# Kernel tuning notes

Measured on AMD Instinct MI355X. Metric: run time of the kernel, lower is better.

The kernel has to match this reference:

```python
import jax, jax.numpy as jnp
import numpy as np

# Instant-NGP hash grid constants (match init_kwargs)
N_MAX, N_MIN = 2048.0, 16.0
L, T, F, DIM = 16, 2**19, 2, 3
NV = 2**DIM  # 8 corners of a voxel
# primes stored as int32 in the original (2654435761 wraps negative) -> replicate exactly
PIS = jnp.asarray(np.array([1, 2654435761, 805459861], dtype=np.uint32).astype(np.int32))
# bin_mask[v, d] = True -> corner v takes floor along dim d
_neigs = np.arange(NV, dtype=np.int64)[:, None]
_dims = np.arange(DIM, dtype=np.int64)[None, :]
BIN_MASK = jnp.asarray((_neigs & (1 << _dims)) == 0)  # [8, 3]
# per-level grid resolutions N_l = N_min * b**l
_b = np.exp((np.log(N_MAX) - np.log(N_MIN)) / L)
SCALES = jnp.asarray((N_MIN * _b ** np.arange(L)).astype(np.float32))  # [L]


def setup_inputs() -> dict:
    key = jax.random.key(0)
    k1, k2 = jax.random.split(key)
    N = 2_000_000
    x = jax.random.uniform(k1, (N, DIM), dtype=jnp.float32)  # points in [0,1)^3 (mu=0, sigma=1)
    # per-level embedding tables, init U(-1e-4, 1e-4) as in the torch module
    W = jax.random.uniform(k2, (L, T, F), minval=-1e-4, maxval=1e-4, dtype=jnp.float32)
    return {"x": x, "W": W}


def _hash(idxs):
    # idxs: [N, 8, 3] int32. int32 wraparound multiply matches low 32 bits of the
    # torch int64 product; since T is a power of two and Python-style mod of a
    # negative by a positive only depends on the low log2(T) bits, result matches.
    prod = idxs * PIS  # [N, 8, 3] int32 (wraps)
    h = prod[..., 0] ^ prod[..., 1] ^ prod[..., 2]
    return h % T  # jnp remainder follows sign of divisor -> nonnegative


def _encode(x, W):
    def level(carry, level_args):
        scale, Wl = level_args
        un_x = x * scale                                   # [N, 3]
        x0 = un_x.astype(jnp.int32)                        # trunc == floor for x >= 0
        diff = jax.lax.stop_gradient(un_x - x0.astype(un_x.dtype))  # [N, 3], detached as in torch
        # corner integer coords: floor where bin_mask else floor+1
        idxs = jnp.where(BIN_MASK[None], x0[:, None, :], x0[:, None, :] + 1)  # [N, 8, 3]
        fv = Wl[_hash(idxs)]                               # [N, 8, F] gather
        wts = jnp.where(BIN_MASK[None], 1.0 - diff[:, None, :], diff[:, None, :])
        wts = wts.prod(axis=-1, keepdims=True)             # [N, 8, 1] trilinear weights
        return carry, (fv * wts).sum(axis=-2)              # [N, F]

    _, ys = jax.lax.scan(level, 0, (SCALES, W))            # [L, N, F]
    # original writes level l into y[:, l*F:(l+1)*F]
    return jnp.transpose(ys, (1, 0, 2)).reshape(x.shape[0], L * F)


def reference(x, W):
    return _encode(x, W)
```

## Files before the change

kernel.cpp:

```cpp
#include <hip/hip_runtime.h>
#include <hip/hip_fp16.h>
#include <math.h>

#define NLEV 16
#define NDENSE 5
#define TBLN (1u << 19)
#define TMASK (TBLN - 1u)
#define NPT 4
#define PR1 2654435761u
#define PR2 805459861u

typedef float f32x4 __attribute__((ext_vector_type(4)));
typedef unsigned int u32;
typedef unsigned int u32x2 __attribute__((ext_vector_type(2)));
typedef unsigned int u32x4 __attribute__((ext_vector_type(4)));

struct ScaleArgs { float s[NLEV]; };

#define DD0 18
#define DD1 23
#define DD2 31
#define DD3 41
#define DD4 55
#define DO0 0
#define DO1 5508
#define DO2 17146
#define DO3 45976
#define DO4 113216
#define DTOT 276566

static __device__ __forceinline__ u32 packf2(float a, float b) {
    __half2 h = __floats2half2_rn(a, b);
    return __builtin_bit_cast(u32, h);
}
static __device__ __forceinline__ float2 unpack16(u32 u) {
    __half2 h = __builtin_bit_cast(__half2, u);
    return __half22float2(h);
}

__global__ __launch_bounds__(256)
void convert_w(const float* __restrict__ W, u32* __restrict__ Wh, int np4)
{
    int i = blockIdx.x * blockDim.x + threadIdx.x;
    if (i >= np4) return;
    const f32x4* src = reinterpret_cast<const f32x4*>(W) + (size_t)i * 2;
    f32x4 A = __builtin_nontemporal_load(src);
    f32x4 B = __builtin_nontemporal_load(src + 1);
    u32x4 o = { packf2(A.x, A.y), packf2(A.z, A.w),
                packf2(B.x, B.y), packf2(B.z, B.w) };
    __builtin_nontemporal_store(o, reinterpret_cast<u32x4*>(Wh) + i);
}

__global__ __launch_bounds__(256)
void build_dense(const float* __restrict__ Wlf, u32x2* __restrict__ Gpl, int D, int P)
{
    int v = blockIdx.x * blockDim.x + threadIdx.x;
    if (v >= P) return;
    int Dx = D - 1;
    int ix = v % Dx;
    int rest = v / Dx;
    int iy = rest % D;
    int iz = rest / D;
    u32 e = ((u32)iy * PR1) ^ ((u32)iz * PR2);
    u32 h0 = (e ^ (u32)ix) & TMASK;
    u32 h1 = (e ^ (u32)(ix + 1)) & TMASK;
    float2 f0 = *reinterpret_cast<const float2*>(Wlf + (size_t)h0 * 2u);
    float2 f1 = *reinterpret_cast<const float2*>(Wlf + (size_t)h1 * 2u);
    u32x2 o = { packf2(f0.x, f0.y), packf2(f1.x, f1.y) };
    Gpl[v] = o;
}


template<int D>
static __device__ __forceinline__ void dense_body(
    const float* __restrict__ x, const u32x2* __restrict__ Gp,
    u32* __restrict__ scl, float scale, int N, int TOT, int t)
{
    constexpr int Dx = D - 1;
    constexpr int zstep = D * Dx;

    int nn[NPT];
    float dx[NPT], dy[NPT], dz[NPT];
    int base[NPT];
    u32x2 P0[NPT], P1[NPT], P2[NPT], P3[NPT];

    #pragma unroll
    for (int i = 0; i < NPT; ++i) {
        int n = t + i * TOT;
        if (n > N - 1) n = N - 1;
        nn[i] = n;
        float px = __builtin_nontemporal_load(&x[(size_t)n * 3 + 0]);
        float py = __builtin_nontemporal_load(&x[(size_t)n * 3 + 1]);
        float pz = __builtin_nontemporal_load(&x[(size_t)n * 3 + 2]);
        float ux = px * scale, uy = py * scale, uz = pz * scale;
        int ix = (int)ux, iy = (int)uy, iz = (int)uz;
        dx[i] = ux - (float)ix;
        dy[i] = uy - (float)iy;
        dz[i] = uz - (float)iz;
        base[i] = (iz * D + iy) * Dx + ix;
    }

    #pragma unroll
    for (int i = 0; i < NPT; ++i) {
        int b = base[i];
        P0[i] = Gp[b];
        P1[i] = Gp[b + Dx];
        P2[i] = Gp[b + zstep];
        P3[i] = Gp[b + zstep + Dx];
    }

    #pragma unroll
    for (int i = 0; i < NPT; ++i) {
        float ax = 0.f, ay = 0.f;
        float wxl = 1.f - dx[i], wxh = dx[i];
        float wyl = 1.f - dy[i], wyh = dy[i];
        float wzl = 1.f - dz[i], wzh = dz[i];
        {
            float2 f0 = unpack16(P0[i].x), f1 = unpack16(P0[i].y);
            float w0 = (wxl * wyl) * wzl, w1 = (wxh * wyl) * wzl;
            ax = fmaf(f0.x, w0, ax); ay = fmaf(f0.y, w0, ay);
            ax = fmaf(f1.x, w1, ax); ay = fmaf(f1.y, w1, ay);
        }
        {
            float2 f0 = unpack16(P1[i].x), f1 = unpack16(P1[i].y);
            float w0 = (wxl * wyh) * wzl, w1 = (wxh * wyh) * wzl;
            ax = fmaf(f0.x, w0, ax); ay = fmaf(f0.y, w0, ay);
            ax = fmaf(f1.x, w1, ax); ay = fmaf(f1.y, w1, ay);
        }
        {
            float2 f0 = unpack16(P2[i].x), f1 = unpack16(P2[i].y);
            float w0 = (wxl * wyl) * wzh, w1 = (wxh * wyl) * wzh;
            ax = fmaf(f0.x, w0, ax); ay = fmaf(f0.y, w0, ay);
            ax = fmaf(f1.x, w1, ax); ay = fmaf(f1.y, w1, ay);
        }
        {
            float2 f0 = unpack16(P3[i].x), f1 = unpack16(P3[i].y);
            float w0 = (wxl * wyh) * wzh, w1 = (wxh * wyh) * wzh;
            ax = fmaf(f0.x, w0, ax); ay = fmaf(f0.y, w0, ay);
            ax = fmaf(f1.x, w1, ax); ay = fmaf(f1.y, w1, ay);
        }
        __builtin_nontemporal_store(packf2(ax, ay), scl + nn[i]);
    }
}

static __device__ __forceinline__ void hash_body(
    const float* __restrict__ x, const u32* __restrict__ Wl,
    u32* __restrict__ scl, float scale, int N, int TOT, int t)
{
    int nn[NPT];
    float dx[NPT], dy[NPT], dz[NPT];
    u32 a0[NPT], a1[NPT], a2[NPT];
    u32 fv[NPT][8];

    #pragma unroll
    for (int i = 0; i < NPT; ++i) {
        int n = t + i * TOT;
        if (n > N - 1) n = N - 1;
        nn[i] = n;
        float px = __builtin_nontemporal_load(&x[(size_t)n * 3 + 0]);
        float py = __builtin_nontemporal_load(&x[(size_t)n * 3 + 1]);
        float pz = __builtin_nontemporal_load(&x[(size_t)n * 3 + 2]);
        float ux = px * scale, uy = py * scale, uz = pz * scale;
        int ix = (int)ux, iy = (int)uy, iz = (int)uz;
        dx[i] = ux - (float)ix;
        dy[i] = uy - (float)iy;
        dz[i] = uz - (float)iz;
        a0[i] = (unsigned)ix;
        a1[i] = (unsigned)iy * PR1;
        a2[i] = (unsigned)iz * PR2;
    }

    #pragma unroll
    for (int i = 0; i < NPT; ++i) {
        u32 b0 = a0[i] + 1u, b1 = a1[i] + PR1, b2 = a2[i] + PR2;
        u32 E[4] = { a1[i] ^ a2[i], b1 ^ a2[i], a1[i] ^ b2, b1 ^ b2 };
        if ((a0[i] & 1u) == 0u) {
            #pragma unroll
            for (int j = 0; j < 4; ++j) {
                u32 hl = (E[j] ^ a0[i]) & TMASK;
                u32x2 p = *reinterpret_cast<const u32x2*>(Wl + (hl & ~1u));
                u32 lo = (hl & 1u) ? p.y : p.x;
                u32 hi = (hl & 1u) ? p.x : p.y;
                fv[i][2 * j + 0] = lo;
                fv[i][2 * j + 1] = hi;
            }
        } else {
            #pragma unroll
            for (int j = 0; j < 4; ++j) {
                u32 hl = (E[j] ^ a0[i]) & TMASK;
                u32 hh = (E[j] ^ b0) & TMASK;
                fv[i][2 * j + 0] = Wl[hl];
                fv[i][2 * j + 1] = Wl[hh];
            }
        }
    }

    #pragma unroll
    for (int i = 0; i < NPT; ++i) {
        float ax = 0.f, ay = 0.f;
        #pragma unroll
        for (int v = 0; v < 8; ++v) {
            float wx = (v & 1) ? dx[i] : 1.f - dx[i];
            float wy = (v & 2) ? dy[i] : 1.f - dy[i];
            float wz = (v & 4) ? dz[i] : 1.f - dz[i];
            float w = (wx * wy) * wz;
            float2 f = unpack16(fv[i][v]);
            ax = fmaf(f.x, w, ax);
            ay = fmaf(f.y, w, ay);
        }
        __builtin_nontemporal_store(packf2(ax, ay), scl + nn[i]);
    }
}

__global__ __launch_bounds__(256)
void fused_levels(const float* __restrict__ x, const u32* __restrict__ Wh,
                  const u32x2* __restrict__ Gp, u32* __restrict__ scratch,
                  ScaleArgs sc, int N, int TOT, int BPL)
{
    int lvl = blockIdx.x / BPL;
    int t = (blockIdx.x - lvl * BPL) * blockDim.x + threadIdx.x;
    if (t >= TOT) return;
    float scale = sc.s[lvl];
    u32* scl = scratch + (size_t)lvl * (size_t)N;

    switch (lvl) {
        case 0: dense_body<DD0>(x, Gp + DO0, scl, scale, N, TOT, t); break;
        case 1: dense_body<DD1>(x, Gp + DO1, scl, scale, N, TOT, t); break;
        case 2: dense_body<DD2>(x, Gp + DO2, scl, scale, N, TOT, t); break;
        case 3: dense_body<DD3>(x, Gp + DO3, scl, scale, N, TOT, t); break;
        case 4: dense_body<DD4>(x, Gp + DO4, scl, scale, N, TOT, t); break;
        default:
            hash_body(x, Wh + (size_t)(lvl - NDENSE) * TBLN, scl, scale, N, TOT, t);
            break;
    }
}

__global__ __launch_bounds__(256)
void transpose_kernel(const u32* __restrict__ sc, float* __restrict__ out, int N)
{
    int n = blockIdx.x * blockDim.x + threadIdx.x;
    if (n >= N) return;
    float r[2 * NLEV];
    #pragma unroll
    for (int l = 0; l < NLEV; ++l) {
        u32 u = __builtin_nontemporal_load(sc + (size_t)l * N + n);
        float2 f = unpack16(u);
        r[2 * l + 0] = f.x;
        r[2 * l + 1] = f.y;
    }
    f32x4* o = reinterpret_cast<f32x4*>(out + (size_t)n * (2 * NLEV));
    #pragma unroll
    for (int j = 0; j < 8; ++j) {
        f32x4 v = { r[4 * j + 0], r[4 * j + 1], r[4 * j + 2], r[4 * j + 3] };
        o[j] = v;
    }
}

__global__ __launch_bounds__(256)
void hashenc_fallback(const float* __restrict__ x, const float* __restrict__ W,
                      float* __restrict__ out, ScaleArgs sc, int N)
{
    int n = blockIdx.x * blockDim.x + threadIdx.x;
    if (n >= N) return;
    float px = x[(size_t)n * 3 + 0];
    float py = x[(size_t)n * 3 + 1];
    float pz = x[(size_t)n * 3 + 2];
    float acc[2 * NLEV];
    #pragma unroll
    for (int l = 0; l < NLEV; ++l) {
        float s = sc.s[l];
        float ux = px * s, uy = py * s, uz = pz * s;
        int ix = (int)ux, iy = (int)uy, iz = (int)uz;
        float dx = ux - (float)ix, dy = uy - (float)iy, dz = uz - (float)iz;
        unsigned a0 = (unsigned)ix;
        unsigned a1 = (unsigned)iy * PR1;
        unsigned a2 = (unsigned)iz * PR2;
        unsigned b0 = a0 + 1u, b1 = a1 + PR1, b2 = a2 + PR2;
        const float* Wl = W + (size_t)l * TBLN * 2u;
        float ax = 0.f, ay = 0.f;
        #pragma unroll
        for (int v = 0; v < 8; ++v) {
            unsigned h = ((v & 1) ? b0 : a0) ^ ((v & 2) ? b1 : a1) ^ ((v & 4) ? b2 : a2);
            h &= TMASK;
            float wx = (v & 1) ? dx : 1.f - dx;
            float wy = (v & 2) ? dy : 1.f - dy;
            float wz = (v & 4) ? dz : 1.f - dz;
            float w = (wx * wy) * wz;
            const float2 fvv = *reinterpret_cast<const float2*>(Wl + (size_t)h * 2u);
            ax = fmaf(fvv.x, w, ax);
            ay = fmaf(fvv.y, w, ay);
        }
        acc[2 * l + 0] = ax;
        acc[2 * l + 1] = ay;
    }
    float4* o = reinterpret_cast<float4*>(out + (size_t)n * (2 * NLEV));
    #pragma unroll
    for (int j = 0; j < 8; ++j)
        o[j] = make_float4(acc[4 * j + 0], acc[4 * j + 1], acc[4 * j + 2], acc[4 * j + 3]);
}

extern "C" void kernel_launch(void* const* d_in, const int* in_sizes, int n_in,
                              void* d_out, int out_size, void* d_ws, size_t ws_size,
                              hipStream_t stream) {
    const float* x = (const float*)d_in[0];
    const float* W = (const float*)d_in[1];
    float* out = (float*)d_out;
    int N = in_sizes[0] / 3;

    ScaleArgs sc;
    double b = exp((log(2048.0) - log(16.0)) / 16.0);
    for (int l = 0; l < NLEV; ++l) {
        double p;
        switch (l) {
            case 0: p = 1.0; break;
            case 1: p = b;   break;
            case 2: p = b * b; break;
            default: p = pow(b, (double)l); break;
        }
        sc.s[l] = (float)(16.0 * p);
    }

    size_t wh_u32 = (size_t)(NLEV - NDENSE) * TBLN;
    size_t gp_u32 = (size_t)DTOT * 2u;
    size_t scr_u32 = (size_t)NLEV * (size_t)N;
    size_t need = (wh_u32 + gp_u32 + scr_u32) * sizeof(u32);

    if (ws_size >= need) {
        u32* Wh = (u32*)d_ws;
        u32x2* Gp = reinterpret_cast<u32x2*>(Wh + wh_u32);
        u32* scratch = Wh + wh_u32 + gp_u32;

        int np4 = (int)(wh_u32 / 4);
        hipLaunchKernelGGL(convert_w, dim3((np4 + 255) / 256), dim3(256), 0, stream,
                           W + (size_t)NDENSE * TBLN * 2u, Wh, np4);

        const int Dl[NDENSE] = { DD0, DD1, DD2, DD3, DD4 };
        const int Ol[NDENSE] = { DO0, DO1, DO2, DO3, DO4 };
        for (int l = 0; l < NDENSE; ++l) {
            int P = (Dl[l] - 1) * Dl[l] * Dl[l];
            hipLaunchKernelGGL(build_dense, dim3((P + 255) / 256), dim3(256), 0, stream,
                               W + (size_t)l * TBLN * 2u, Gp + Ol[l], Dl[l], P);
        }

        int TOT = (N + NPT - 1) / NPT;
        int BPL = (TOT + 255) / 256;
        hipLaunchKernelGGL(fused_levels, dim3(NLEV * BPL), dim3(256), 0, stream,
                           x, Wh, Gp, scratch, sc, N, TOT, BPL);

        int gt = (N + 255) / 256;
        hipLaunchKernelGGL(transpose_kernel, dim3(gt), dim3(256), 0, stream,
                           scratch, out, N);
    } else {
        int grid = (N + 255) / 256;
        hipLaunchKernelGGL(hashenc_fallback, dim3(grid), dim3(256), 0, stream,
                           x, W, out, sc, N);
    }
}
```

Before: 687.3 us.

## Serve coarse levels from LDS-resident grids, densify level 5, tile transpose through LDS

Levels 0 and 1 now get separate kernels that copy a small dense fp16 grid (18^3 and 23^3 entries) into shared memory and do the trilinear lookups from LDS. Level 5 (D=75) becomes a precomputed dense paired grid instead of going through the hash table. The transpose kernel stages each level's scratch values in LDS so the 32-float output rows are written coalesced. These changes aim to reduce scattered global gathers and uncoalesced writes, at the cost of two extra launches that each re-read x and a larger dense-grid build.

```diff
diff --git a/kernel.cpp b/kernel.cpp
--- a/kernel.cpp
+++ b/kernel.cpp
@@ -3,10 +3,10 @@
 #include <math.h>
 
 #define NLEV 16
-#define NDENSE 5
 #define TBLN (1u << 19)
 #define TMASK (TBLN - 1u)
 #define NPT 4
+#define NPTL 16
 #define PR1 2654435761u
 #define PR2 805459861u
 
@@ -17,17 +17,20 @@
 
 struct ScaleArgs { float s[NLEV]; };
 
-#define DD0 18
-#define DD1 23
+#define DU0 18
+#define DU1 23
+#define GU0 0
+#define GU1 5832
+#define GUTOT 17999
 #define DD2 31
 #define DD3 41
 #define DD4 55
-#define DO0 0
-#define DO1 5508
-#define DO2 17146
-#define DO3 45976
-#define DO4 113216
-#define DTOT 276566
+#define DD5 75
+#define GO2 0
+#define GO3 28830
+#define GO4 96070
+#define GO5 259420
+#define GPTOT 675670
 
 static __device__ __forceinline__ u32 packf2(float a, float b) {
     __half2 h = __floats2half2_rn(a, b);
@@ -49,6 +52,20 @@
     u32x4 o = { packf2(A.x, A.y), packf2(A.z, A.w),
                 packf2(B.x, B.y), packf2(B.z, B.w) };
     __builtin_nontemporal_store(o, reinterpret_cast<u32x4*>(Wh) + i);
+}
+
+__global__ __launch_bounds__(256)
+void build_unpaired(const float* __restrict__ Wlf, u32* __restrict__ Gu, int D, int P)
+{
+    int v = blockIdx.x * blockDim.x + threadIdx.x;
+    if (v >= P) return;
+    int ix = v % D;
+    int rest = v / D;
+    int iy = rest % D;
+    int iz = rest / D;
+    u32 h = (((u32)iy * PR1) ^ ((u32)iz * PR2) ^ (u32)ix) & TMASK;
+    float2 f = *reinterpret_cast<const float2*>(Wlf + (size_t)h * 2u);
+    Gu[v] = packf2(f.x, f.y);
 }
 
 __global__ __launch_bounds__(256)
@@ -68,6 +85,49 @@
     float2 f1 = *reinterpret_cast<const float2*>(Wlf + (size_t)h1 * 2u);
     u32x2 o = { packf2(f0.x, f0.y), packf2(f1.x, f1.y) };
     Gpl[v] = o;
+}
+
+template<int D>
+__global__ __launch_bounds__(256)
+void lds_level(const float* __restrict__ x, const u32* __restrict__ Gu,
+               u32* __restrict__ scl, float scale, int N)
+{
+    __shared__ u32 g[D * D * D];
+    for (int i = threadIdx.x; i < D * D * D; i += 256) g[i] = Gu[i];
+    __syncthreads();
+
+    int base = blockIdx.x * (256 * NPTL);
+    #pragma unroll 4
+    for (int i = 0; i < NPTL; ++i) {
+        int n = base + i * 256 + (int)threadIdx.x;
+        if (n < N) {
+            float px = __builtin_nontemporal_load(&x[(size_t)n * 3 + 0]);
+            float py = __builtin_nontemporal_load(&x[(size_t)n * 3 + 1]);
+            float pz = __builtin_nontemporal_load(&x[(size_t)n * 3 + 2]);
+            float ux = px * scale, uy = py * scale, uz = pz * scale;
+            int ix = (int)ux, iy = (int)uy, iz = (int)uz;
+            float dx = ux - (float)ix, dy = uy - (float)iy, dz = uz - (float)iz;
+            int b = (iz * D + iy) * D + ix;
+            u32 c0 = g[b],             c1 = g[b + 1];
+            u32 c2 = g[b + D],         c3 = g[b + D + 1];
+            u32 c4 = g[b + D * D],     c5 = g[b + D * D + 1];
+            u32 c6 = g[b + D * D + D], c7 = g[b + D * D + D + 1];
+            float wxl = 1.f - dx, wxh = dx;
+            float wyl = 1.f - dy, wyh = dy;
+            float wzl = 1.f - dz, wzh = dz;
+            float ax = 0.f, ay = 0.f;
+            float2 f;
+            f = unpack16(c0); { float w = (wxl * wyl) * wzl; ax = fmaf(f.x, w, ax); ay = fmaf(f.y, w, ay); }
+            f = unpack16(c1); { float w = (wxh * wyl) * wzl; ax = fmaf(f.x, w, ax); ay = fmaf(f.y, w, ay); }
+            f = unpack16(c2); { float w = (wxl * wyh) * wzl; ax = fmaf(f.x, w, ax); ay = fmaf(f.y, w, ay); }
+            f = unpack16(c3); { float w = (wxh * wyh) * wzl; ax = fmaf(f.x, w, ax); ay = fmaf(f.y, w, ay); }
+            f = unpack16(c4); { float w = (wxl * wyl) * wzh; ax = fmaf(f.x, w, ax); ay = fmaf(f.y, w, ay); }
+            f = unpack16(c5); { float w = (wxh * wyl) * wzh; ax = fmaf(f.x, w, ax); ay = fmaf(f.y, w, ay); }
+            f = unpack16(c6); { float w = (wxl * wyh) * wzh; ax = fmaf(f.x, w, ax); ay = fmaf(f.y, w, ay); }
+            f = unpack16(c7); { float w = (wxh * wyh) * wzh; ax = fmaf(f.x, w, ax); ay = fmaf(f.y, w, ay); }
+            __builtin_nontemporal_store(packf2(ax, ay), scl + n);
+        }
+    }
 }
 
 
@@ -217,20 +277,20 @@
                   const u32x2* __restrict__ Gp, u32* __restrict__ scratch,
                   ScaleArgs sc, int N, int TOT, int BPL)
 {
-    int lvl = blockIdx.x / BPL;
-    int t = (blockIdx.x - lvl * BPL) * blockDim.x + threadIdx.x;
+    int li = blockIdx.x / BPL;
+    int lvl = li + 2;
+    int t = (blockIdx.x - li * BPL) * blockDim.x + threadIdx.x;
     if (t >= TOT) return;
     float scale = sc.s[lvl];
     u32* scl = scratch + (size_t)lvl * (size_t)N;
 
     switch (lvl) {
-        case 0: dense_body<DD0>(x, Gp + DO0, scl, scale, N, TOT, t); break;
-        case 1: dense_body<DD1>(x, Gp + DO1, scl, scale, N, TOT, t); break;
-        case 2: dense_body<DD2>(x, Gp + DO2, scl, scale, N, TOT, t); break;
-        case 3: dense_body<DD3>(x, Gp + DO3, scl, scale, N, TOT, t); break;
-        case 4: dense_body<DD4>(x, Gp + DO4, scl, scale, N, TOT, t); break;
+        case 2: dense_body<DD2>(x, Gp + GO2, scl, scale, N, TOT, t); break;
+        case 3: dense_body<DD3>(x, Gp + GO3, scl, scale, N, TOT, t); break;
+        case 4: dense_body<DD4>(x, Gp + GO4, scl, scale, N, TOT, t); break;
+        case 5: dense_body<DD5>(x, Gp + GO5, scl, scale, N, TOT, t); break;
         default:
-            hash_body(x, Wh + (size_t)(lvl - NDENSE) * TBLN, scl, scale, N, TOT, t);
+            hash_body(x, Wh + (size_t)(lvl - 6) * TBLN, scl, scale, N, TOT, t);
             break;
     }
 }
@@ -238,21 +298,27 @@
 __global__ __launch_bounds__(256)
 void transpose_kernel(const u32* __restrict__ sc, float* __restrict__ out, int N)
 {
-    int n = blockIdx.x * blockDim.x + threadIdx.x;
-    if (n >= N) return;
-    float r[2 * NLEV];
+    __shared__ u32 lds[16][257];
+    int P0 = blockIdx.x * 256;
+    int t = threadIdx.x;
     #pragma unroll
     for (int l = 0; l < NLEV; ++l) {
-        u32 u = __builtin_nontemporal_load(sc + (size_t)l * N + n);
-        float2 f = unpack16(u);
-        r[2 * l + 0] = f.x;
-        r[2 * l + 1] = f.y;
-    }
-    f32x4* o = reinterpret_cast<f32x4*>(out + (size_t)n * (2 * NLEV));
-    #pragma unroll
-    for (int j = 0; j < 8; ++j) {
-        f32x4 v = { r[4 * j + 0], r[4 * j + 1], r[4 * j + 2], r[4 * j + 3] };
-        o[j] = v;
+        int n = P0 + t;
+        if (n < N) lds[l][t] = __builtin_nontemporal_load(sc + (size_t)l * N + n);
+    }
+    __syncthreads();
+    int w = t >> 6, l6 = t & 63;
+    #pragma unroll
+    for (int k = 0; k < 8; ++k) {
+        int p = w * 64 + k * 8 + (l6 >> 3);
+        int c = l6 & 7;
+        if (P0 + p < N) {
+            float2 f0 = unpack16(lds[2 * c][p]);
+            float2 f1 = unpack16(lds[2 * c + 1][p]);
+            f32x4 v = { f0.x, f0.y, f1.x, f1.y };
+            __builtin_nontemporal_store(v,
+                reinterpret_cast<f32x4*>(out + (size_t)(P0 + p) * 32u + (size_t)c * 4u));
+        }
     }
 }
 
@@ -320,31 +386,51 @@
         sc.s[l] = (float)(16.0 * p);
     }
 
-    size_t wh_u32 = (size_t)(NLEV - NDENSE) * TBLN;
-    size_t gp_u32 = (size_t)DTOT * 2u;
+    size_t wh_u32 = (size_t)(NLEV - 6) * TBLN;
+    size_t gp_u32 = (size_t)GPTOT * 2u;
+    size_t gu_u32 = (size_t)GUTOT;
     size_t scr_u32 = (size_t)NLEV * (size_t)N;
-    size_t need = (wh_u32 + gp_u32 + scr_u32) * sizeof(u32);
+    size_t need = (wh_u32 + gp_u32 + gu_u32 + scr_u32) * sizeof(u32);
 
     if (ws_size >= need) {
         u32* Wh = (u32*)d_ws;
         u32x2* Gp = reinterpret_cast<u32x2*>(Wh + wh_u32);
-        u32* scratch = Wh + wh_u32 + gp_u32;
+        u32* Gu = Wh + wh_u32 + gp_u32;
+        u32* scratch = Gu + gu_u32;
 
         int np4 = (int)(wh_u32 / 4);
         hipLaunchKernelGGL(convert_w, dim3((np4 + 255) / 256), dim3(256), 0, stream,
-                           W + (size_t)NDENSE * TBLN * 2u, Wh, np4);
-
-        const int Dl[NDENSE] = { DD0, DD1, DD2, DD3, DD4 };
-        const int Ol[NDENSE] = { DO0, DO1, DO2, DO3, DO4 };
-        for (int l = 0; l < NDENSE; ++l) {
-            int P = (Dl[l] - 1) * Dl[l] * Dl[l];
+                           W + (size_t)6 * TBLN * 2u, Wh, np4);
+
+        {
+            int P0c = DU0 * DU0 * DU0;
+            hipLaunchKernelGGL(build_unpaired, dim3((P0c + 255) / 256), dim3(256), 0, stream,
+                               W + 0, Gu + GU0, DU0, P0c);
+            int P1c = DU1 * DU1 * DU1;
+            hipLaunchKernelGGL(build_unpaired, dim3((P1c + 255) / 256), dim3(256), 0, stream,
+                               W + (size_t)1 * TBLN * 2u, Gu + GU1, DU1, P1c);
+        }
+
+        const int Dl[4] = { DD2, DD3, DD4, DD5 };
+        const int Ol[4] = { GO2, GO3, GO4, GO5 };
+        for (int i = 0; i < 4; ++i) {
+            int l = 2 + i;
+            int P = (Dl[i] - 1) * Dl[i] * Dl[i];
             hipLaunchKernelGGL(build_dense, dim3((P + 255) / 256), dim3(256), 0, stream,
-                               W + (size_t)l * TBLN * 2u, Gp + Ol[l], Dl[l], P);
+                               W + (size_t)l * TBLN * 2u, Gp + Ol[i], Dl[i], P);
+        }
+
+        {
+            int blocks = (N + 256 * NPTL - 1) / (256 * NPTL);
+            hipLaunchKernelGGL(lds_level<DU0>, dim3(blocks), dim3(256), 0, stream,
+                               x, Gu + GU0, scratch + 0, sc.s[0], N);
+            hipLaunchKernelGGL(lds_level<DU1>, dim3(blocks), dim3(256), 0, stream,
+                               x, Gu + GU1, scratch + (size_t)N, sc.s[1], N);
         }
 
         int TOT = (N + NPT - 1) / NPT;
         int BPL = (TOT + 255) / 256;
-        hipLaunchKernelGGL(fused_levels, dim3(NLEV * BPL), dim3(256), 0, stream,
+        hipLaunchKernelGGL(fused_levels, dim3(14 * BPL), dim3(256), 0, stream,
                            x, Wh, Gp, scratch, sc, N, TOT, BPL);
 
         int gt = (N + 255) / 256;
```

New measurement: 636.1 us. -7.4%, faster.
